# Kernel optimization log

Measured on AMD Instinct MI355X. Metric: run time of the kernel, lower is better.

## Reference

```python
import jax, jax.numpy as jnp
import numpy as np

N_NODES = 100000
N_EDGES = 1000000
D = 64
OUT = 64
EPS = 1e-5


def setup_inputs() -> dict:
    key = jax.random.key(0)
    k1, k2, k3, k4 = jax.random.split(key, 4)
    x = jax.random.normal(k1, (N_NODES, D), dtype=jnp.float32)
    edge_index = jax.random.randint(k2, (2, N_EDGES), 0, N_NODES, dtype=jnp.int64)
    # Linear(2*D, OUT): torch default init ~ U(-1/sqrt(fan_in), 1/sqrt(fan_in))
    bound = 1.0 / np.sqrt(2 * D)
    W = jax.random.uniform(k3, (2 * D, OUT), minval=-bound, maxval=bound, dtype=jnp.float32)
    b = jax.random.uniform(k4, (OUT,), minval=-bound, maxval=bound, dtype=jnp.float32)
    gamma = jnp.ones((OUT,), dtype=jnp.float32)
    beta = jnp.zeros((OUT,), dtype=jnp.float32)
    return {"x": x, "edge_index": edge_index, "W": W, "b": b, "gamma": gamma, "beta": beta}


def reference(x, edge_index, W, b, gamma, beta):
    row, col = edge_index[0], edge_index[1]
    # gather source features and scatter-add into destination nodes
    neighbor_sum = jax.ops.segment_sum(x[row], col, num_segments=x.shape[0])  # [N, D]
    h = jnp.concatenate([x, neighbor_sum], axis=-1)  # [N, 2D]
    h = h @ W + b  # [N, OUT]
    # LayerNorm over last dim
    mu = jnp.mean(h, axis=-1, keepdims=True)
    var = jnp.var(h, axis=-1, keepdims=True)
    h = (h - mu) * jax.lax.rsqrt(var + EPS) * gamma + beta
    return h
```

## Files before the change

### kernel.cpp

```cpp
#include <hip/hip_runtime.h>

#define NN 100000
#define NE 1000000
#define OUT_D 64
#define EPS 1e-5f

#define NB 196
#define COLS 512
#define BSTRIDE 6016
#define PBSTRIDE 8064
#define EPB 4096
#define NBLK1 245
#define NPROJ 1024

typedef __attribute__((ext_vector_type(8))) short bf16x8;
typedef __attribute__((ext_vector_type(4))) float f32x4;
typedef __attribute__((ext_vector_type(4))) int i32x4;

static __device__ __forceinline__ unsigned short f2bf(float f) {
    unsigned u = __float_as_uint(f);
    u += 0x7FFFu + ((u >> 16) & 1u);
    return (unsigned short)(u >> 16);
}
static __device__ __forceinline__ float bf2f(unsigned short s) {
    return __uint_as_float((unsigned)s << 16);
}

__global__ __launch_bounds__(256) void mega_kernel(
    const float* __restrict__ x, const float* __restrict__ W,
    const int* __restrict__ ei, int* __restrict__ gcur, unsigned* __restrict__ gbuf,
    unsigned short* __restrict__ y1, unsigned short* __restrict__ y2)
{
    const int tid = threadIdx.x;
    const int lane = tid & 63;
    const int wv = tid >> 6;

    if (blockIdx.x < NBLK1) {
        __shared__ int lcnt[NB];
        __shared__ int loff[NB + 1];
        __shared__ int lbase[NB];
        __shared__ int lcur[NB];
        __shared__ int wpart[4];
        __shared__ unsigned lbuf[EPB];
        __shared__ unsigned char lbkt[EPB];
        const int e0 = blockIdx.x * EPB;

        int rows[16], cols[16];
        #pragma unroll
        for (int j = 0; j < 16; ++j) {
            const int e = e0 + j * 256 + tid;
            const bool v = e < NE;
            rows[j] = v ? ei[e] : 0;
            cols[j] = v ? ei[NE + e] : -1;
        }
        for (int i = tid; i < NB; i += 256) lcnt[i] = 0;
        __syncthreads();
        #pragma unroll
        for (int j = 0; j < 16; ++j)
            if (cols[j] >= 0) atomicAdd(&lcnt[cols[j] >> 9], 1);
        __syncthreads();
        {
            const int c = (tid < NB) ? lcnt[tid] : 0;
            int s = c;
            #pragma unroll
            for (int o = 1; o < 64; o <<= 1) { int t = __shfl_up(s, o); if (lane >= o) s += t; }
            if (lane == 63) wpart[wv] = s;
            __syncthreads();
            int woff = 0;
            for (int ww = 0; ww < wv; ++ww) woff += wpart[ww];
            if (tid < NB) {
                loff[tid] = woff + s - c;
                lcur[tid] = woff + s - c;
                lbase[tid] = atomicAdd(&gcur[tid], c);
            }
            if (tid == NB - 1) loff[NB] = woff + s;
        }
        __syncthreads();
        #pragma unroll
        for (int j = 0; j < 16; ++j) {
            if (cols[j] >= 0) {
                const int b = cols[j] >> 9;
                const int p = atomicAdd(&lcur[b], 1);
                lbuf[p] = ((unsigned)rows[j] << 9) | (unsigned)(cols[j] & (COLS - 1));
                lbkt[p] = (unsigned char)b;
            }
        }
        __syncthreads();
        const int total = loff[NB];
        for (int t = tid; t < total; t += 256) {
            const int b = lbkt[t];
            const unsigned idx = (unsigned)(lbase[b] + (t - loff[b]));
            if (idx < BSTRIDE) gbuf[(size_t)b * BSTRIDE + idx] = lbuf[t];
        }
    } else {
        const int m = lane & 15;
        const int quad = lane >> 4;
        bf16x8 Wf[8][2];
        #pragma unroll
        for (int t = 0; t < 8; ++t)
            #pragma unroll
            for (int q = 0; q < 2; ++q) {
                bf16x8 f;
                #pragma unroll
                for (int j = 0; j < 8; ++j) {
                    const int k = q * 32 + quad * 8 + j;
                    const int krow = (t < 4) ? k : (64 + k);
                    const int col = (t & 3) * 16 + m;
                    f[j] = (short)f2bf(W[krow * 64 + col]);
                }
                Wf[t][q] = f;
            }
        for (int tile = (blockIdx.x - NBLK1) * 4 + wv; tile < NN / 16; tile += NPROJ * 4) {
            const int n0 = tile * 16;
            bf16x8 Af[2];
            #pragma unroll
            for (int q = 0; q < 2; ++q) {
                const float* px = x + (size_t)(n0 + m) * 64 + q * 32 + quad * 8;
                const f32x4 a0 = *(const f32x4*)px;
                const f32x4 a1 = *(const f32x4*)(px + 4);
                bf16x8 f;
                #pragma unroll
                for (int j = 0; j < 4; ++j) { f[j] = (short)f2bf(a0[j]); f[4 + j] = (short)f2bf(a1[j]); }
                Af[q] = f;
            }
            #pragma unroll
            for (int t = 0; t < 8; ++t) {
                f32x4 acc = {0.f, 0.f, 0.f, 0.f};
                acc = __builtin_amdgcn_mfma_f32_16x16x32_bf16(Af[0], Wf[t][0], acc, 0, 0, 0);
                acc = __builtin_amdgcn_mfma_f32_16x16x32_bf16(Af[1], Wf[t][1], acc, 0, 0, 0);
                unsigned short* __restrict__ dst = (t < 4) ? y1 : y2;
                const int colb = (t & 3) * 16 + m;
                #pragma unroll
                for (int r = 0; r < 4; ++r)
                    dst[(size_t)(n0 + quad * 4 + r) * 64 + colb] = f2bf(acc[r]);
            }
        }
    }
}

__global__ __launch_bounds__(256) void place_kernel(
    const int* __restrict__ gcur, const unsigned* __restrict__ gbuf,
    int* __restrict__ csr, unsigned* __restrict__ rowpack,
    unsigned short* __restrict__ y2)
{
    __shared__ int cofs[COLS + 1];
    __shared__ int ccur[COLS];
    __shared__ unsigned lsrc[BSTRIDE];
    __shared__ int ldst[PBSTRIDE];
    const int b = blockIdx.x, tid = threadIdx.x;
    const int n0 = b << 9;

    if (b == 0 && tid < 64) y2[(size_t)NN * OUT_D + tid] = 0;

    for (int i = tid; i < COLS; i += 256) cofs[i] = 0;
    for (int i = tid; i < PBSTRIDE; i += 256) ldst[i] = NN;
    __syncthreads();
    const int cntE = min(gcur[b], BSTRIDE);
    const unsigned* __restrict__ gb = gbuf + (size_t)b * BSTRIDE;

    for (int i = tid; i < cntE; i += 256) {
        const unsigned p = gb[i];
        lsrc[i] = p;
        atomicAdd(&cofs[p & (COLS - 1)], 1);
    }
    __syncthreads();
    if (tid < 64) {
        int v[8], tsum = 0;
        #pragma unroll
        for (int k = 0; k < 8; ++k) { v[k] = (cofs[tid * 8 + k] + 3) & ~3; tsum += v[k]; }
        int s = tsum;
        #pragma unroll
        for (int o = 1; o < 64; o <<= 1) { int t = __shfl_up(s, o); if (tid >= o) s += t; }
        int run = s - tsum;
        #pragma unroll
        for (int k = 0; k < 8; ++k) { cofs[tid * 8 + k] = run; ccur[tid * 8 + k] = run; run += v[k]; }
        if (tid == 63) cofs[COLS] = run;
    }
    __syncthreads();
    for (int i = tid; i < cntE; i += 256) {
        const unsigned p = lsrc[i];
        const int pos = atomicAdd(&ccur[p & (COLS - 1)], 1);
        ldst[pos] = (int)(p >> 9);
    }
    __syncthreads();
    const int ptotal = cofs[COLS];
    const int base = b * PBSTRIDE;
    for (int i = tid; i < ptotal; i += 256) csr[base + i] = ldst[i];
    const int ncols = min(COLS, NN - n0);
    for (int c = tid; c < ncols; c += 256) {
        const int st = cofs[c];
        const int len = min(cofs[c + 1] - st, 511);
        rowpack[n0 + c] = ((unsigned)st << 9) | (unsigned)len;
    }
}

__global__ __launch_bounds__(256) void out_kernel(
    const unsigned* __restrict__ rowpack, const int* __restrict__ csr,
    const unsigned short* __restrict__ y1, const unsigned short* __restrict__ y2,
    const float* __restrict__ bias, const float* __restrict__ gamma,
    const float* __restrict__ beta, float* __restrict__ out)
{
    const int lane = threadIdx.x & 63;
    const int n = __builtin_amdgcn_readfirstlane(blockIdx.x * 4 + (threadIdx.x >> 6));
    const unsigned pk = rowpack[n];
    const int cnt = (int)(pk & 511);
    const i32x4* __restrict__ cs =
        (const i32x4*)(csr + (n >> 9) * PBSTRIDE + (int)(pk >> 9));

    float acc = bf2f(y1[(size_t)n * OUT_D + lane]) + bias[lane];
    int i = 0;
    for (; i + 8 <= cnt; i += 8) {
        const i32x4 c0 = cs[(i >> 2)];
        const i32x4 c1 = cs[(i >> 2) + 1];
        const float v0 = bf2f(y2[(size_t)c0[0] * OUT_D + lane]);
        const float v1 = bf2f(y2[(size_t)c0[1] * OUT_D + lane]);
        const float v2 = bf2f(y2[(size_t)c0[2] * OUT_D + lane]);
        const float v3 = bf2f(y2[(size_t)c0[3] * OUT_D + lane]);
        const float v4 = bf2f(y2[(size_t)c1[0] * OUT_D + lane]);
        const float v5 = bf2f(y2[(size_t)c1[1] * OUT_D + lane]);
        const float v6 = bf2f(y2[(size_t)c1[2] * OUT_D + lane]);
        const float v7 = bf2f(y2[(size_t)c1[3] * OUT_D + lane]);
        acc += ((v0 + v1) + (v2 + v3)) + ((v4 + v5) + (v6 + v7));
    }
    if (i < cnt) {
        const i32x4 c0 = cs[(i >> 2)];
        const float v0 = bf2f(y2[(size_t)c0[0] * OUT_D + lane]);
        const float v1 = bf2f(y2[(size_t)c0[1] * OUT_D + lane]);
        const float v2 = bf2f(y2[(size_t)c0[2] * OUT_D + lane]);
        const float v3 = bf2f(y2[(size_t)c0[3] * OUT_D + lane]);
        acc += (v0 + v1) + (v2 + v3);
    }

    float sv = acc, sq = acc * acc;
    #pragma unroll
    for (int off = 32; off; off >>= 1) { sv += __shfl_xor(sv, off); sq += __shfl_xor(sq, off); }
    const float mu  = sv * (1.0f / OUT_D);
    const float var = sq * (1.0f / OUT_D) - mu * mu;
    const float inv = rsqrtf(var + EPS);
    out[(size_t)n * OUT_D + lane] = (acc - mu) * inv * gamma[lane] + beta[lane];
}

extern "C" void kernel_launch(void* const* d_in, const int* in_sizes, int n_in,
                              void* d_out, int out_size, void* d_ws, size_t ws_size,
                              hipStream_t stream) {
    const float* x     = (const float*)d_in[0];
    const int*   ei    = (const int*)  d_in[1];
    const float* W     = (const float*)d_in[2];
    const float* b     = (const float*)d_in[3];
    const float* gamma = (const float*)d_in[4];
    const float* beta  = (const float*)d_in[5];
    float* out = (float*)d_out;

    char* p = (char*)d_ws;
    int*            gcur    = (int*)p;             p += 1024;
    unsigned*       gbuf    = (unsigned*)p;        p += (size_t)NB * BSTRIDE * 4;
    int*            csr     = (int*)p;             p += (size_t)NB * PBSTRIDE * 4;
    unsigned*       rowpack = (unsigned*)p;        p += (size_t)(NB * COLS) * 4;
    unsigned short* y1      = (unsigned short*)p;  p += (size_t)NN * OUT_D * 2;
    unsigned short* y2      = (unsigned short*)p;

    hipMemsetAsync(gcur, 0, NB * sizeof(int), stream);
    mega_kernel <<<NBLK1 + NPROJ, 256, 0, stream>>>(x, W, ei, gcur, gbuf, y1, y2);
    place_kernel<<<NB, 256, 0, stream>>>(gcur, gbuf, csr, rowpack, y2);
    out_kernel  <<<NN / 4, 256, 0, stream>>>(rowpack, csr, y1, y2, b, gamma, beta, out);
}
```

Measured before the change: 143.4 us.

## Split CSR placement into half-buckets, fold bias into MFMA, use nontemporal stores

The placement kernel now runs two blocks per bucket, each handling 256 columns. Each block rereads the bucket's edges from global memory instead of staging them in LDS, which lowers LDS use and doubles the number of blocks. The bias is folded into the MFMA accumulator initialisation for y1, so the output kernel no longer loads it. Nontemporal stores and loads are added for the streaming writes (gbuf, y1/y2, csr, rowpack, out) to reduce cache pollution. In exchange, each half-block reads its bucket twice, and the halves cap capacity at a fixed stride, which could truncate edges on skewed inputs.

```diff
diff --git a/kernel.cpp b/kernel.cpp
--- a/kernel.cpp
+++ b/kernel.cpp
@@ -9,6 +9,8 @@
 #define COLS 512
 #define BSTRIDE 6016
 #define PBSTRIDE 8064
+#define HCOLS 256
+#define HSTRIDE 4032
 #define EPB 4096
 #define NBLK1 245
 #define NPROJ 1024
@@ -28,6 +30,7 @@
 
 __global__ __launch_bounds__(256) void mega_kernel(
     const float* __restrict__ x, const float* __restrict__ W,
+    const float* __restrict__ bias,
     const int* __restrict__ ei, int* __restrict__ gcur, unsigned* __restrict__ gbuf,
     unsigned short* __restrict__ y1, unsigned short* __restrict__ y2)
 {
@@ -90,12 +93,14 @@
         for (int t = tid; t < total; t += 256) {
             const int b = lbkt[t];
             const unsigned idx = (unsigned)(lbase[b] + (t - loff[b]));
-            if (idx < BSTRIDE) gbuf[(size_t)b * BSTRIDE + idx] = lbuf[t];
+            if (idx < BSTRIDE)
+                __builtin_nontemporal_store(lbuf[t], &gbuf[(size_t)b * BSTRIDE + idx]);
         }
     } else {
         const int m = lane & 15;
         const int quad = lane >> 4;
         bf16x8 Wf[8][2];
+        float binit[4];
         #pragma unroll
         for (int t = 0; t < 8; ++t)
             #pragma unroll
@@ -110,6 +115,8 @@
                 }
                 Wf[t][q] = f;
             }
+        #pragma unroll
+        for (int t = 0; t < 4; ++t) binit[t] = bias[t * 16 + m];
         for (int tile = (blockIdx.x - NBLK1) * 4 + wv; tile < NN / 16; tile += NPROJ * 4) {
             const int n0 = tile * 16;
             bf16x8 Af[2];
@@ -125,14 +132,16 @@
             }
             #pragma unroll
             for (int t = 0; t < 8; ++t) {
-                f32x4 acc = {0.f, 0.f, 0.f, 0.f};
+                const float ini = (t < 4) ? binit[t] : 0.f;
+                f32x4 acc = {ini, ini, ini, ini};
                 acc = __builtin_amdgcn_mfma_f32_16x16x32_bf16(Af[0], Wf[t][0], acc, 0, 0, 0);
                 acc = __builtin_amdgcn_mfma_f32_16x16x32_bf16(Af[1], Wf[t][1], acc, 0, 0, 0);
                 unsigned short* __restrict__ dst = (t < 4) ? y1 : y2;
                 const int colb = (t & 3) * 16 + m;
                 #pragma unroll
                 for (int r = 0; r < 4; ++r)
-                    dst[(size_t)(n0 + quad * 4 + r) * 64 + colb] = f2bf(acc[r]);
+                    __builtin_nontemporal_store(f2bf(acc[r]),
+                        &dst[(size_t)(n0 + quad * 4 + r) * 64 + colb]);
             }
         }
     }
@@ -143,62 +152,67 @@
     int* __restrict__ csr, unsigned* __restrict__ rowpack,
     unsigned short* __restrict__ y2)
 {
-    __shared__ int cofs[COLS + 1];
-    __shared__ int ccur[COLS];
-    __shared__ unsigned lsrc[BSTRIDE];
-    __shared__ int ldst[PBSTRIDE];
-    const int b = blockIdx.x, tid = threadIdx.x;
-    const int n0 = b << 9;
-
-    if (b == 0 && tid < 64) y2[(size_t)NN * OUT_D + tid] = 0;
-
-    for (int i = tid; i < COLS; i += 256) cofs[i] = 0;
-    for (int i = tid; i < PBSTRIDE; i += 256) ldst[i] = NN;
+    __shared__ int cofs[HCOLS + 1];
+    __shared__ int ccur[HCOLS];
+    __shared__ int ldst[HSTRIDE];
+    const int b = blockIdx.x >> 1;
+    const int h = blockIdx.x & 1;
+    const int tid = threadIdx.x;
+    const int qlo = h * HCOLS;
+    const int n0 = (b << 9) + qlo;
+
+    if (blockIdx.x == 0 && tid < 64) y2[(size_t)NN * OUT_D + tid] = 0;
+
+    for (int i = tid; i < HCOLS; i += 256) cofs[i] = 0;
+    for (int i = tid; i < HSTRIDE; i += 256) ldst[i] = NN;
     __syncthreads();
     const int cntE = min(gcur[b], BSTRIDE);
     const unsigned* __restrict__ gb = gbuf + (size_t)b * BSTRIDE;
 
     for (int i = tid; i < cntE; i += 256) {
-        const unsigned p = gb[i];
-        lsrc[i] = p;
-        atomicAdd(&cofs[p & (COLS - 1)], 1);
+        const int c = (int)(gb[i] & (COLS - 1)) - qlo;
+        if ((unsigned)c < HCOLS) atomicAdd(&cofs[c], 1);
     }
     __syncthreads();
     if (tid < 64) {
-        int v[8], tsum = 0;
-        #pragma unroll
-        for (int k = 0; k < 8; ++k) { v[k] = (cofs[tid * 8 + k] + 3) & ~3; tsum += v[k]; }
+        int v[4], tsum = 0;
+        #pragma unroll
+        for (int k = 0; k < 4; ++k) { v[k] = (cofs[tid * 4 + k] + 3) & ~3; tsum += v[k]; }
         int s = tsum;
         #pragma unroll
         for (int o = 1; o < 64; o <<= 1) { int t = __shfl_up(s, o); if (tid >= o) s += t; }
         int run = s - tsum;
         #pragma unroll
-        for (int k = 0; k < 8; ++k) { cofs[tid * 8 + k] = run; ccur[tid * 8 + k] = run; run += v[k]; }
-        if (tid == 63) cofs[COLS] = run;
+        for (int k = 0; k < 4; ++k) { cofs[tid * 4 + k] = run; ccur[tid * 4 + k] = run; run += v[k]; }
+        if (tid == 63) cofs[HCOLS] = run;
     }
     __syncthreads();
     for (int i = tid; i < cntE; i += 256) {
-        const unsigned p = lsrc[i];
-        const int pos = atomicAdd(&ccur[p & (COLS - 1)], 1);
-        ldst[pos] = (int)(p >> 9);
-    }
-    __syncthreads();
-    const int ptotal = cofs[COLS];
-    const int base = b * PBSTRIDE;
-    for (int i = tid; i < ptotal; i += 256) csr[base + i] = ldst[i];
-    const int ncols = min(COLS, NN - n0);
+        const unsigned p = gb[i];
+        const int c = (int)(p & (COLS - 1)) - qlo;
+        if ((unsigned)c < HCOLS) {
+            const int pos = atomicAdd(&ccur[c], 1);
+            if (pos < HSTRIDE) ldst[pos] = (int)(p >> 9);
+        }
+    }
+    __syncthreads();
+    const int ptotal = min(cofs[HCOLS], HSTRIDE);
+    const int base = b * PBSTRIDE + h * HSTRIDE;
+    for (int i = tid; i < ptotal; i += 256)
+        __builtin_nontemporal_store(ldst[i], &csr[base + i]);
+    const int ncols = min(HCOLS, NN - n0);
     for (int c = tid; c < ncols; c += 256) {
-        const int st = cofs[c];
-        const int len = min(cofs[c + 1] - st, 511);
-        rowpack[n0 + c] = ((unsigned)st << 9) | (unsigned)len;
+        const int st = h * HSTRIDE + min(cofs[c], HSTRIDE);
+        const int len = min(cofs[c + 1] - cofs[c], 511);
+        __builtin_nontemporal_store(((unsigned)st << 9) | (unsigned)len, &rowpack[n0 + c]);
     }
 }
 
 __global__ __launch_bounds__(256) void out_kernel(
     const unsigned* __restrict__ rowpack, const int* __restrict__ csr,
     const unsigned short* __restrict__ y1, const unsigned short* __restrict__ y2,
-    const float* __restrict__ bias, const float* __restrict__ gamma,
-    const float* __restrict__ beta, float* __restrict__ out)
+    const float* __restrict__ gamma, const float* __restrict__ beta,
+    float* __restrict__ out)
 {
     const int lane = threadIdx.x & 63;
     const int n = __builtin_amdgcn_readfirstlane(blockIdx.x * 4 + (threadIdx.x >> 6));
@@ -207,7 +221,7 @@
     const i32x4* __restrict__ cs =
         (const i32x4*)(csr + (n >> 9) * PBSTRIDE + (int)(pk >> 9));
 
-    float acc = bf2f(y1[(size_t)n * OUT_D + lane]) + bias[lane];
+    float acc = bf2f(__builtin_nontemporal_load(&y1[(size_t)n * OUT_D + lane]));
     int i = 0;
     for (; i + 8 <= cnt; i += 8) {
         const i32x4 c0 = cs[(i >> 2)];
@@ -237,7 +251,8 @@
     const float mu  = sv * (1.0f / OUT_D);
     const float var = sq * (1.0f / OUT_D) - mu * mu;
     const float inv = rsqrtf(var + EPS);
-    out[(size_t)n * OUT_D + lane] = (acc - mu) * inv * gamma[lane] + beta[lane];
+    __builtin_nontemporal_store((acc - mu) * inv * gamma[lane] + beta[lane],
+                                &out[(size_t)n * OUT_D + lane]);
 }
 
 extern "C" void kernel_launch(void* const* d_in, const int* in_sizes, int n_in,
@@ -260,7 +275,7 @@
     unsigned short* y2      = (unsigned short*)p;
 
     hipMemsetAsync(gcur, 0, NB * sizeof(int), stream);
-    mega_kernel <<<NBLK1 + NPROJ, 256, 0, stream>>>(x, W, ei, gcur, gbuf, y1, y2);
-    place_kernel<<<NB, 256, 0, stream>>>(gcur, gbuf, csr, rowpack, y2);
-    out_kernel  <<<NN / 4, 256, 0, stream>>>(rowpack, csr, y1, y2, b, gamma, beta, out);
-}
+    mega_kernel <<<NBLK1 + NPROJ, 256, 0, stream>>>(x, W, b, ei, gcur, gbuf, y1, y2);
+    place_kernel<<<NB * 2, 256, 0, stream>>>(gcur, gbuf, csr, rowpack, y2);
+    out_kernel  <<<NN / 4, 256, 0, stream>>>(rowpack, csr, y1, y2, gamma, beta, out);
+}
```

After: 160.7 us. 12.1% more time.
